# Performance work log

Measured on AMD Instinct MI355X. Metric: run time of the kernel, lower is better.

## Reference

```python
import jax, jax.numpy as jnp
import numpy as np

N, H, E = 40000, 128, 640000
BN_EPS = 1e-5


def setup_inputs() -> dict:
    key = jax.random.key(0)
    ks = jax.random.split(key, 5)
    x = jax.random.normal(ks[0], (N, H), dtype=jnp.float32)
    edge_index = jax.random.randint(ks[1], (2, E), 0, N, dtype=jnp.int64)
    eps = jnp.zeros((1,), dtype=jnp.float32)
    s = 1.0 / np.sqrt(H)  # torch Linear init scale
    W1 = jax.random.uniform(ks[2], (H, H), jnp.float32, -s, s)
    b1 = jnp.zeros((H,), dtype=jnp.float32)
    W2 = jax.random.uniform(ks[3], (H, H), jnp.float32, -s, s)
    b2 = jnp.zeros((H,), dtype=jnp.float32)
    gamma = jnp.ones((H,), dtype=jnp.float32)
    beta = jnp.zeros((H,), dtype=jnp.float32)
    return {"x": x, "edge_index": edge_index, "eps": eps,
            "W1": W1, "b1": b1, "W2": W2, "b2": b2,
            "gamma": gamma, "beta": beta}


def reference(x, edge_index, eps, W1, b1, W2, b2, gamma, beta):
    src = edge_index[0]
    tgt = edge_index[1]
    # gather source features, scatter-add into target rows: [N, H]
    agg = jax.ops.segment_sum(x[src], tgt, num_segments=x.shape[0])
    out = agg + (1.0 + eps) * x
    # MLP: Linear -> ReLU -> Linear -> BatchNorm1d (train mode) -> ReLU
    h = jax.nn.relu(out @ W1.T + b1)
    h = h @ W2.T + b2
    mean = jnp.mean(h, axis=0)
    var = jnp.mean((h - mean) ** 2, axis=0)  # biased var, as BN uses
    h = (h - mean) * jax.lax.rsqrt(var + BN_EPS) * gamma + beta
    return jax.nn.relu(h)
```

## Files before the change

### kernel.cpp

```cpp
#include <hip/hip_runtime.h>

#define HDIM 128
#define BN_EPS 1e-5f
#define SCAN_BINS 1024
#define NPART 8
#define LSTR 136

typedef short short8 __attribute__((ext_vector_type(8)));
typedef float floatx4 __attribute__((ext_vector_type(4)));

__device__ __forceinline__ unsigned short f2b(float f) {
    union { float f; unsigned u; } v; v.f = f;
    unsigned r = v.u + 0x7FFFu + ((v.u >> 16) & 1u);
    return (unsigned short)(r >> 16);
}

__device__ __forceinline__ float b2f(unsigned short b) {
    union { unsigned u; float f; } v; v.u = (unsigned)b << 16;
    return v.f;
}

__global__ __launch_bounds__(256) void prep_kernel(
    const float* __restrict__ x, unsigned short* __restrict__ xB, long n4,
    const float* __restrict__ W1, const float* __restrict__ W2,
    unsigned short* __restrict__ W1B, unsigned short* __restrict__ W2B,
    const int* __restrict__ eidx, int* __restrict__ hist,
    int* __restrict__ rank, int E)
{
    int tid = blockIdx.x * 256 + threadIdx.x;
    int stride = gridDim.x * 256;
    for (long i = tid; i < n4; i += stride) {
        float4 v = ((const float4*)x)[i];
        ushort4 o;
        o.x = f2b(v.x); o.y = f2b(v.y); o.z = f2b(v.z); o.w = f2b(v.w);
        ((ushort4*)xB)[i] = o;
    }
    for (int i = tid; i < HDIM * HDIM; i += stride) {
        W1B[i] = f2b(W1[i]);
        W2B[i] = f2b(W2[i]);
    }
    for (int e = tid; e < E; e += stride) {
        rank[e] = atomicAdd(&hist[eidx[E + e]], 1);
    }
}

__global__ __launch_bounds__(256) void block_scan_kernel(
    const int* __restrict__ hist, int* __restrict__ offsets,
    int* __restrict__ blockSums, float* __restrict__ statSum, int N)
{
    __shared__ int ts[256];
    int b = blockIdx.x, t = threadIdx.x;
    if (b == 0 && t < 2 * HDIM) statSum[t] = 0.f;
    int base = b * SCAN_BINS + t * 4;
    int4 h = make_int4(0, 0, 0, 0);
    if (base + 3 < N) {
        h = *(const int4*)(hist + base);
    } else {
        if (base + 0 < N) h.x = hist[base + 0];
        if (base + 1 < N) h.y = hist[base + 1];
        if (base + 2 < N) h.z = hist[base + 2];
    }
    int s = h.x + h.y + h.z + h.w;
    ts[t] = s;
    __syncthreads();
    for (int off = 1; off < 256; off <<= 1) {
        int v = ts[t];
        int add = (t >= off) ? ts[t - off] : 0;
        __syncthreads();
        ts[t] = v + add;
        __syncthreads();
    }
    int excl = ts[t] - s;
    int4 o;
    o.x = excl;
    o.y = o.x + h.x;
    o.z = o.y + h.y;
    o.w = o.z + h.z;
    if (base + 3 < N) {
        *(int4*)(offsets + base) = o;
    } else {
        if (base + 0 < N) offsets[base + 0] = o.x;
        if (base + 1 < N) offsets[base + 1] = o.y;
        if (base + 2 < N) offsets[base + 2] = o.z;
    }
    if (t == 255) blockSums[b] = ts[255];
}

__global__ __launch_bounds__(256) void scan_finalize_kernel(
    const int* __restrict__ blockSums, int* __restrict__ offsets, int N, int NB)
{
    __shared__ int ts[256];
    int b = blockIdx.x, t = threadIdx.x;
    ts[t] = (t < NB) ? blockSums[t] : 0;
    __syncthreads();
    for (int off = 1; off < 256; off <<= 1) {
        int v = ts[t];
        int add = (t >= off) ? ts[t - off] : 0;
        __syncthreads();
        ts[t] = v + add;
        __syncthreads();
    }
    int prefix = (b == 0) ? 0 : ts[b - 1];
    if (b == 0 && t == 0) offsets[N] = ts[NB - 1];
    int base = b * SCAN_BINS + t * 4;
    if (base + 3 < N) {
        int4 o = *(int4*)(offsets + base);
        o.x += prefix; o.y += prefix; o.z += prefix; o.w += prefix;
        *(int4*)(offsets + base) = o;
    } else {
        for (int j = 0; j < 4; j++) {
            int i = base + j;
            if (i < N) offsets[i] += prefix;
        }
    }
}

__global__ __launch_bounds__(256) void reorder_kernel(
    const int* __restrict__ eidx, const int* __restrict__ offsets,
    const int* __restrict__ rank, int* __restrict__ srcSorted,
    int E, int partSize)
{
    int part = blockIdx.x & (NPART - 1);
    int bi = blockIdx.x >> 3;
    int nb = gridDim.x >> 3;
    int lo = part * partSize;
    int hi = lo + partSize;
    int stride = nb * 256;
    for (int e = bi * 256 + threadIdx.x; e < E; e += stride) {
        int t = eidx[E + e];
        if (t >= lo && t < hi) {
            srcSorted[offsets[t] + rank[e]] = eidx[e];
        }
    }
}

__global__ __launch_bounds__(256, 4) void mega_kernel(
    const float* __restrict__ x, const unsigned short* __restrict__ xB,
    const int* __restrict__ offsets, const int* __restrict__ srcSorted,
    const float* __restrict__ eps,
    const unsigned short* __restrict__ W1B, const float* __restrict__ b1,
    const unsigned short* __restrict__ W2B, const float* __restrict__ b2,
    float* __restrict__ out, float* __restrict__ statSum,
    float* __restrict__ statSqs, int N)
{
    __shared__ unsigned short sT[64 * LSTR];
    __shared__ float sSum[HDIM];
    __shared__ float sSqs[HDIM];

    int tid = threadIdx.x;
    int rb = blockIdx.x * 64;
    if (tid < HDIM) { sSum[tid] = 0.f; sSqs[tid] = 0.f; }

    float coef = 1.0f + eps[0];
    int tx = tid & 15, ty = tid >> 4;
    int col = tx * 8;
    for (int g = 0; g < 4; g++) {
        int r = g * 16 + ty;
        int row = rb + r;
        float acc[8] = {0.f, 0.f, 0.f, 0.f, 0.f, 0.f, 0.f, 0.f};
        if (row < N) {
            float4 xv0 = *(const float4*)(x + (size_t)row * HDIM + col);
            float4 xv1 = *(const float4*)(x + (size_t)row * HDIM + col + 4);
            acc[0] = coef * xv0.x; acc[1] = coef * xv0.y;
            acc[2] = coef * xv0.z; acc[3] = coef * xv0.w;
            acc[4] = coef * xv1.x; acc[5] = coef * xv1.y;
            acc[6] = coef * xv1.z; acc[7] = coef * xv1.w;
            int beg = offsets[row], end = offsets[row + 1];
            int e = beg;
            for (; e + 7 < end; e += 8) {
                short8 u[8];
                #pragma unroll
                for (int q = 0; q < 8; q++) {
                    int s = srcSorted[e + q];
                    u[q] = *(const short8*)(xB + (size_t)s * HDIM + col);
                }
                #pragma unroll
                for (int q = 0; q < 8; q++)
                    #pragma unroll
                    for (int j = 0; j < 8; j++)
                        acc[j] += b2f((unsigned short)u[q][j]);
            }
            for (; e < end; e++) {
                int s = srcSorted[e];
                short8 u = *(const short8*)(xB + (size_t)s * HDIM + col);
                #pragma unroll
                for (int j = 0; j < 8; j++)
                    acc[j] += b2f((unsigned short)u[j]);
            }
        }
        short8 o;
        #pragma unroll
        for (int j = 0; j < 8; j++) o[j] = (short)f2b(acc[j]);
        *(short8*)(sT + r * LSTR + col) = o;
    }
    __syncthreads();

    int w = tid >> 6;
    int l = tid & 63;
    int m = l & 15, quad = l >> 4;
    unsigned short* myT = sT + w * 16 * LSTR;

    floatx4 acc1[8];
    #pragma unroll
    for (int t = 0; t < 8; t++) acc1[t] = (floatx4){0.f, 0.f, 0.f, 0.f};
    #pragma unroll
    for (int kk = 0; kk < 4; kk++) {
        int k0 = kk * 32 + quad * 8;
        short8 a = *(const short8*)(myT + m * LSTR + k0);
        #pragma unroll
        for (int t = 0; t < 8; t++) {
            short8 bfr = *(const short8*)(W1B + (size_t)(t * 16 + m) * HDIM + k0);
            acc1[t] = __builtin_amdgcn_mfma_f32_16x16x32_bf16(a, bfr, acc1[t], 0, 0, 0);
        }
    }
    #pragma unroll
    for (int t = 0; t < 8; t++) {
        int colc = t * 16 + m;
        float bs = b1[colc];
        #pragma unroll
        for (int r = 0; r < 4; r++) {
            float v = fmaxf(acc1[t][r] + bs, 0.f);
            myT[(quad * 4 + r) * LSTR + colc] = f2b(v);
        }
    }

    floatx4 acc2[8];
    #pragma unroll
    for (int t = 0; t < 8; t++) acc2[t] = (floatx4){0.f, 0.f, 0.f, 0.f};
    #pragma unroll
    for (int kk = 0; kk < 4; kk++) {
        int k0 = kk * 32 + quad * 8;
        short8 a = *(const short8*)(myT + m * LSTR + k0);
        #pragma unroll
        for (int t = 0; t < 8; t++) {
            short8 bfr = *(const short8*)(W2B + (size_t)(t * 16 + m) * HDIM + k0);
            acc2[t] = __builtin_amdgcn_mfma_f32_16x16x32_bf16(a, bfr, acc2[t], 0, 0, 0);
        }
    }
    int row0 = rb + w * 16 + quad * 4;
    #pragma unroll
    for (int t = 0; t < 8; t++) {
        int colc = t * 16 + m;
        float bs = b2[colc];
        float cs = 0.f, cq = 0.f;
        #pragma unroll
        for (int r = 0; r < 4; r++) {
            int row = row0 + r;
            if (row < N) {
                float v = acc2[t][r] + bs;
                out[(size_t)row * HDIM + colc] = v;
                cs += v; cq += v * v;
            }
        }
        cs += __shfl_xor(cs, 16, 64);
        cs += __shfl_xor(cs, 32, 64);
        cq += __shfl_xor(cq, 16, 64);
        cq += __shfl_xor(cq, 32, 64);
        if (quad == 0) {
            atomicAdd(&sSum[colc], cs);
            atomicAdd(&sSqs[colc], cq);
        }
    }
    __syncthreads();
    if (tid < HDIM) {
        atomicAdd(&statSum[tid], sSum[tid]);
        atomicAdd(&statSqs[tid], sSqs[tid]);
    }
}

__global__ __launch_bounds__(256) void bn_apply_kernel(
    float* __restrict__ out, const float* __restrict__ statSum,
    const float* __restrict__ statSqs, const float* __restrict__ gamma,
    const float* __restrict__ beta, int N, long n4)
{
    __shared__ float sSc[HDIM];
    __shared__ float sSh[HDIM];
    int t = threadIdx.x;
    if (t < HDIM) {
        float invN = 1.0f / (float)N;
        float mean = statSum[t] * invN;
        float var = statSqs[t] * invN - mean * mean;
        float sc = gamma[t] * rsqrtf(var + BN_EPS);
        sSc[t] = sc;
        sSh[t] = beta[t] - mean * sc;
    }
    __syncthreads();
    long stride = (long)gridDim.x * 256;
    for (long i = (long)blockIdx.x * 256 + t; i < n4; i += stride) {
        int cg = (int)(i & 31) * 4;
        float4 v = ((float4*)out)[i];
        v.x = fmaxf(v.x * sSc[cg + 0] + sSh[cg + 0], 0.f);
        v.y = fmaxf(v.y * sSc[cg + 1] + sSh[cg + 1], 0.f);
        v.z = fmaxf(v.z * sSc[cg + 2] + sSh[cg + 2], 0.f);
        v.w = fmaxf(v.w * sSc[cg + 3] + sSh[cg + 3], 0.f);
        ((float4*)out)[i] = v;
    }
}

extern "C" void kernel_launch(void* const* d_in, const int* in_sizes, int n_in,
                              void* d_out, int out_size, void* d_ws, size_t ws_size,
                              hipStream_t stream) {
    const float* x     = (const float*)d_in[0];
    const int*   eidx  = (const int*)d_in[1];
    const float* eps   = (const float*)d_in[2];
    const float* W1    = (const float*)d_in[3];
    const float* b1    = (const float*)d_in[4];
    const float* W2    = (const float*)d_in[5];
    const float* b2    = (const float*)d_in[6];
    const float* gamma = (const float*)d_in[7];
    const float* beta  = (const float*)d_in[8];
    float* out = (float*)d_out;

    int N = in_sizes[0] / HDIM;
    int E = in_sizes[1] / 2;
    size_t NH = (size_t)N * HDIM;
    int NB = (N + SCAN_BINS - 1) / SCAN_BINS;
    int NpadOff = (N + 1 + 3) & ~3;
    int partSize = (N + NPART - 1) / NPART;
    long n4 = (long)NH / 4;

    unsigned short* xB   = (unsigned short*)d_ws;
    unsigned short* W1B  = xB + NH;
    unsigned short* W2B  = W1B + HDIM * HDIM;
    float* statSum = (float*)(W2B + HDIM * HDIM);
    float* statSqs = statSum + HDIM;
    int*   hist    = (int*)(statSqs + HDIM);
    int*   offsets = hist + N;
    int*   rank    = offsets + NpadOff;
    int*   srcSorted = rank + E;
    int*   blockSums = srcSorted + E;

    hipMemsetAsync(hist, 0, (size_t)N * sizeof(int), stream);
    prep_kernel<<<1280, 256, 0, stream>>>(x, xB, n4, W1, W2, W1B, W2B, eidx, hist, rank, E);
    block_scan_kernel<<<NB, 256, 0, stream>>>(hist, offsets, blockSums, statSum, N);
    scan_finalize_kernel<<<NB, 256, 0, stream>>>(blockSums, offsets, N, NB);
    reorder_kernel<<<2048, 256, 0, stream>>>(eidx, offsets, rank, srcSorted, E, partSize);
    int gblocks = (N + 63) / 64;
    mega_kernel<<<gblocks, 256, 0, stream>>>(
        x, xB, offsets, srcSorted, eps, W1B, b1, W2B, b2,
        out, statSum, statSqs, N);
    bn_apply_kernel<<<2048, 256, 0, stream>>>(
        out, statSum, statSqs, gamma, beta, N, n4);
}
```

Before: 198.8 us.

## Shrink mega_kernel tiles to 16 rows, split MLP columns across waves, replicate BN stats

Each mega_kernel block now handles 16 rows instead of 64, so there are four times as many blocks, and it declares a higher occupancy target. The four waves now split the 128 output columns of both GEMMs between them instead of each taking its own 16 rows, which needs an extra barrier between layers. BN statistics are accumulated with direct global atomics into 8 replicated buffers, and bn_apply sums those buffers. A 4-wide tail loop is added to the gather. The aim is better latency hiding and load balance in the gather, at the cost of four times as many global atomic adds.

```diff
diff --git a/kernel.cpp b/kernel.cpp
--- a/kernel.cpp
+++ b/kernel.cpp
@@ -5,6 +5,8 @@
 #define SCAN_BINS 1024
 #define NPART 8
 #define LSTR 136
+#define MROWS 16
+#define NREP 8
 
 typedef short short8 __attribute__((ext_vector_type(8)));
 typedef float floatx4 __attribute__((ext_vector_type(4)));
@@ -50,7 +52,9 @@
 {
     __shared__ int ts[256];
     int b = blockIdx.x, t = threadIdx.x;
-    if (b == 0 && t < 2 * HDIM) statSum[t] = 0.f;
+    if (b == 0) {
+        for (int i = t; i < 2 * NREP * HDIM; i += 256) statSum[i] = 0.f;
+    }
     int base = b * SCAN_BINS + t * 4;
     int4 h = make_int4(0, 0, 0, 0);
     if (base + 3 < N) {
@@ -134,7 +138,7 @@
     }
 }
 
-__global__ __launch_bounds__(256, 4) void mega_kernel(
+__global__ __launch_bounds__(256, 8) void mega_kernel(
     const float* __restrict__ x, const unsigned short* __restrict__ xB,
     const int* __restrict__ offsets, const int* __restrict__ srcSorted,
     const float* __restrict__ eps,
@@ -143,20 +147,17 @@
     float* __restrict__ out, float* __restrict__ statSum,
     float* __restrict__ statSqs, int N)
 {
-    __shared__ unsigned short sT[64 * LSTR];
-    __shared__ float sSum[HDIM];
-    __shared__ float sSqs[HDIM];
+    __shared__ unsigned short sA[MROWS * LSTR];
+    __shared__ unsigned short sH[MROWS * LSTR];
 
     int tid = threadIdx.x;
-    int rb = blockIdx.x * 64;
-    if (tid < HDIM) { sSum[tid] = 0.f; sSqs[tid] = 0.f; }
+    int rb = blockIdx.x * MROWS;
 
     float coef = 1.0f + eps[0];
     int tx = tid & 15, ty = tid >> 4;
     int col = tx * 8;
-    for (int g = 0; g < 4; g++) {
-        int r = g * 16 + ty;
-        int row = rb + r;
+    {
+        int row = rb + ty;
         float acc[8] = {0.f, 0.f, 0.f, 0.f, 0.f, 0.f, 0.f, 0.f};
         if (row < N) {
             float4 xv0 = *(const float4*)(x + (size_t)row * HDIM + col);
@@ -180,6 +181,19 @@
                     for (int j = 0; j < 8; j++)
                         acc[j] += b2f((unsigned short)u[q][j]);
             }
+            for (; e + 3 < end; e += 4) {
+                short8 u[4];
+                #pragma unroll
+                for (int q = 0; q < 4; q++) {
+                    int s = srcSorted[e + q];
+                    u[q] = *(const short8*)(xB + (size_t)s * HDIM + col);
+                }
+                #pragma unroll
+                for (int q = 0; q < 4; q++)
+                    #pragma unroll
+                    for (int j = 0; j < 8; j++)
+                        acc[j] += b2f((unsigned short)u[q][j]);
+            }
             for (; e < end; e++) {
                 int s = srcSorted[e];
                 short8 u = *(const short8*)(xB + (size_t)s * HDIM + col);
@@ -191,56 +205,59 @@
         short8 o;
         #pragma unroll
         for (int j = 0; j < 8; j++) o[j] = (short)f2b(acc[j]);
-        *(short8*)(sT + r * LSTR + col) = o;
+        *(short8*)(sA + ty * LSTR + col) = o;
     }
     __syncthreads();
 
     int w = tid >> 6;
     int l = tid & 63;
     int m = l & 15, quad = l >> 4;
-    unsigned short* myT = sT + w * 16 * LSTR;
-
-    floatx4 acc1[8];
-    #pragma unroll
-    for (int t = 0; t < 8; t++) acc1[t] = (floatx4){0.f, 0.f, 0.f, 0.f};
+    int cbase = w * 32;
+
+    floatx4 acc1[2];
+    #pragma unroll
+    for (int t = 0; t < 2; t++) acc1[t] = (floatx4){0.f, 0.f, 0.f, 0.f};
     #pragma unroll
     for (int kk = 0; kk < 4; kk++) {
         int k0 = kk * 32 + quad * 8;
-        short8 a = *(const short8*)(myT + m * LSTR + k0);
-        #pragma unroll
-        for (int t = 0; t < 8; t++) {
-            short8 bfr = *(const short8*)(W1B + (size_t)(t * 16 + m) * HDIM + k0);
+        short8 a = *(const short8*)(sA + m * LSTR + k0);
+        #pragma unroll
+        for (int t = 0; t < 2; t++) {
+            short8 bfr = *(const short8*)(W1B + (size_t)(cbase + t * 16 + m) * HDIM + k0);
             acc1[t] = __builtin_amdgcn_mfma_f32_16x16x32_bf16(a, bfr, acc1[t], 0, 0, 0);
         }
     }
     #pragma unroll
-    for (int t = 0; t < 8; t++) {
-        int colc = t * 16 + m;
+    for (int t = 0; t < 2; t++) {
+        int colc = cbase + t * 16 + m;
         float bs = b1[colc];
         #pragma unroll
         for (int r = 0; r < 4; r++) {
             float v = fmaxf(acc1[t][r] + bs, 0.f);
-            myT[(quad * 4 + r) * LSTR + colc] = f2b(v);
-        }
-    }
-
-    floatx4 acc2[8];
-    #pragma unroll
-    for (int t = 0; t < 8; t++) acc2[t] = (floatx4){0.f, 0.f, 0.f, 0.f};
+            sH[(quad * 4 + r) * LSTR + colc] = f2b(v);
+        }
+    }
+    __syncthreads();
+
+    floatx4 acc2[2];
+    #pragma unroll
+    for (int t = 0; t < 2; t++) acc2[t] = (floatx4){0.f, 0.f, 0.f, 0.f};
     #pragma unroll
     for (int kk = 0; kk < 4; kk++) {
         int k0 = kk * 32 + quad * 8;
-        short8 a = *(const short8*)(myT + m * LSTR + k0);
-        #pragma unroll
-        for (int t = 0; t < 8; t++) {
-            short8 bfr = *(const short8*)(W2B + (size_t)(t * 16 + m) * HDIM + k0);
+        short8 a = *(const short8*)(sH + m * LSTR + k0);
+        #pragma unroll
+        for (int t = 0; t < 2; t++) {
+            short8 bfr = *(const short8*)(W2B + (size_t)(cbase + t * 16 + m) * HDIM + k0);
             acc2[t] = __builtin_amdgcn_mfma_f32_16x16x32_bf16(a, bfr, acc2[t], 0, 0, 0);
         }
     }
-    int row0 = rb + w * 16 + quad * 4;
-    #pragma unroll
-    for (int t = 0; t < 8; t++) {
-        int colc = t * 16 + m;
+    float* repSum = statSum + (blockIdx.x & (NREP - 1)) * HDIM;
+    float* repSqs = statSqs + (blockIdx.x & (NREP - 1)) * HDIM;
+    int row0 = rb + quad * 4;
+    #pragma unroll
+    for (int t = 0; t < 2; t++) {
+        int colc = cbase + t * 16 + m;
         float bs = b2[colc];
         float cs = 0.f, cq = 0.f;
         #pragma unroll
@@ -257,14 +274,9 @@
         cq += __shfl_xor(cq, 16, 64);
         cq += __shfl_xor(cq, 32, 64);
         if (quad == 0) {
-            atomicAdd(&sSum[colc], cs);
-            atomicAdd(&sSqs[colc], cq);
-        }
-    }
-    __syncthreads();
-    if (tid < HDIM) {
-        atomicAdd(&statSum[tid], sSum[tid]);
-        atomicAdd(&statSqs[tid], sSqs[tid]);
+            atomicAdd(&repSum[colc], cs);
+            atomicAdd(&repSqs[colc], cq);
+        }
     }
 }
 
@@ -277,9 +289,15 @@
     __shared__ float sSh[HDIM];
     int t = threadIdx.x;
     if (t < HDIM) {
+        float s = 0.f, q = 0.f;
+        #pragma unroll
+        for (int r = 0; r < NREP; r++) {
+            s += statSum[r * HDIM + t];
+            q += statSqs[r * HDIM + t];
+        }
         float invN = 1.0f / (float)N;
-        float mean = statSum[t] * invN;
-        float var = statSqs[t] * invN - mean * mean;
+        float mean = s * invN;
+        float var = q * invN - mean * mean;
         float sc = gamma[t] * rsqrtf(var + BN_EPS);
         sSc[t] = sc;
         sSh[t] = beta[t] - mean * sc;
@@ -323,8 +341,8 @@
     unsigned short* W1B  = xB + NH;
     unsigned short* W2B  = W1B + HDIM * HDIM;
     float* statSum = (float*)(W2B + HDIM * HDIM);
-    float* statSqs = statSum + HDIM;
-    int*   hist    = (int*)(statSqs + HDIM);
+    float* statSqs = statSum + NREP * HDIM;
+    int*   hist    = (int*)(statSqs + NREP * HDIM);
     int*   offsets = hist + N;
     int*   rank    = offsets + NpadOff;
     int*   srcSorted = rank + E;
@@ -335,7 +353,7 @@
     block_scan_kernel<<<NB, 256, 0, stream>>>(hist, offsets, blockSums, statSum, N);
     scan_finalize_kernel<<<NB, 256, 0, stream>>>(blockSums, offsets, N, NB);
     reorder_kernel<<<2048, 256, 0, stream>>>(eidx, offsets, rank, srcSorted, E, partSize);
-    int gblocks = (N + 63) / 64;
+    int gblocks = (N + MROWS - 1) / MROWS;
     mega_kernel<<<gblocks, 256, 0, stream>>>(
         x, xB, offsets, srcSorted, eps, W1B, b1, W2B, b2,
         out, statSum, statSqs, N);
```

After: 184.1 us. -7.4%, faster.
